# Performance work log

Hardware: AMD Instinct MI355X
Metric: run time of the kernel (lower is better)

Reference implementation:

```python
import jax, jax.numpy as jnp
import numpy as np

N_Q, N_K = 4096, 32768
D_IN_Q, D_IN_V = 1024, 1024
D_QK, D_V = 512, 512
MASK_VAL = -1000.0


def setup_inputs() -> dict:
    key = jax.random.key(0)
    ks = jax.random.split(key, 9)
    X1 = jax.random.normal(ks[0], (N_Q, D_IN_Q), dtype=jnp.float32)
    X2 = jax.random.normal(ks[1], (N_K, D_IN_V), dtype=jnp.float32)
    row_map = jax.random.randint(ks[2], (N_K,), 0, N_Q, dtype=jnp.int32)
    # Linear params (stored as (in, out) for x @ W + b), xavier-ish scale
    def lin(k, din, dout):
        s = jnp.sqrt(6.0 / (din + dout)).astype(jnp.float32)
        return jax.random.uniform(k, (din, dout), jnp.float32, -s, s)
    Wq = lin(ks[3], D_IN_Q, D_QK); bq = jnp.zeros((D_QK,), jnp.float32)
    Wk = lin(ks[4], D_IN_V, D_QK); bk = jnp.zeros((D_QK,), jnp.float32)
    Wv = lin(ks[5], D_IN_V, D_V); bv = jnp.zeros((D_V,), jnp.float32)
    return {"X1": X1, "X2": X2, "Wq": Wq, "bq": bq, "Wk": Wk, "bk": bk,
            "Wv": Wv, "bv": bv, "row_map": row_map}


def reference(X1, X2, Wq, bq, Wk, bk, Wv, bv, row_map):
    n_q = X1.shape[0]
    n_k = X2.shape[0]
    Q = X1 @ Wq + bq                      # (n_q, d_qk)
    K = X2 @ Wk + bk                      # (n_k, d_qk)
    V = X2 @ Wv + bv                      # (n_k, d_v)
    scale = 1.0 / jnp.sqrt(jnp.float32(Q.shape[1]))
    S = (Q @ K.T) * scale                 # (n_q, n_k)
    cols = jnp.arange(n_k)
    # Keep only entries (row_map[j], j); everything else set to -1000 (as in torch)
    S_masked = jnp.full_like(S, MASK_VAL).at[row_map, cols].set(S[row_map, cols])
    W = jax.nn.softmax(S_masked, axis=1)  # (n_q, n_k)
    C = W @ V                             # (n_q, d_v)
    # Queries with no related keys get zero rows (torch skips them entirely)
    counts = jax.ops.segment_sum(jnp.ones((n_k,), jnp.float32), row_map,
                                 num_segments=n_q)
    return jnp.where(counts[:, None] > 0, C, jnp.zeros_like(C))
```

## Files before the change

### kernel.cpp

```cpp
#include <hip/hip_runtime.h>

typedef unsigned short bhalf;
typedef __bf16 bf16x8 __attribute__((ext_vector_type(8)));
typedef float f32x4 __attribute__((ext_vector_type(4)));

#define NQ 4096
#define NK 32768
#define DIN 1024
#define DQK 512
#define CAP 64
#define SCALE 0.044194173824159216f

__device__ __forceinline__ unsigned f2bf(float f) {
  union { float f; unsigned u; } c; c.f = f;
  unsigned u = c.u;
  return (u + 0x7fffu + ((u >> 16) & 1u)) >> 16;
}
__device__ __forceinline__ float bf_lo(unsigned u) {
  union { unsigned u; float f; } c; c.u = u << 16; return c.f;
}
__device__ __forceinline__ float bf_hi(unsigned u) {
  union { unsigned u; float f; } c; c.u = u & 0xffff0000u; return c.f;
}

__global__ __launch_bounds__(256) void prep_kernel(
    const float* __restrict__ Wq, const float* __restrict__ Wk,
    const float* __restrict__ Wv, const float* __restrict__ bq,
    const float* __restrict__ X1, const int* __restrict__ rm,
    bhalf* __restrict__ Wq_b, bhalf* __restrict__ Wk_b, bhalf* __restrict__ WvT,
    bhalf* __restrict__ X1_b,
    float* __restrict__ g_s, int* __restrict__ cnt, int* __restrict__ keyslot) {
  __shared__ float tile[32][33];
  const int b = blockIdx.x;
  const int tid = threadIdx.x;
  if (b < 512) {
    const int bx = b & 15, by = b >> 4;
    const int tx = tid & 31, ty = tid >> 5;
    const int x = bx * 32 + tx;
#pragma unroll
    for (int yy = 0; yy < 32; yy += 8)
      tile[ty + yy][tx] = Wv[(size_t)(by * 32 + ty + yy) * 512 + x];
    __syncthreads();
    const int k = by * 32 + tx;
#pragma unroll
    for (int yy = 0; yy < 32; yy += 8)
      WvT[(size_t)(bx * 32 + ty + yy) * 1024 + k] = (bhalf)f2bf(tile[tx][ty + yy]);
  } else if (b < 768) {
    const int w = (b - 512) * 4 + (tid >> 6);
    const int lane = tid & 63;
    const float* row = Wk + (size_t)w * 512;
    float s = 0.f;
#pragma unroll
    for (int t = 0; t < 2; t++) {
      float4 a = *(const float4*)(row + t * 256 + lane * 4);
      float4 bb2 = *(const float4*)(bq + t * 256 + lane * 4);
      s += a.x * bb2.x + a.y * bb2.y + a.z * bb2.z + a.w * bb2.w;
    }
#pragma unroll
    for (int d = 32; d; d >>= 1) s += __shfl_xor(s, d);
    if (lane == 0) g_s[w] = s * SCALE;
  } else if (b < 1792) {
    const float* in; bhalf* out; int idx;
    if (b < 1280) { in = Wq; out = Wq_b; idx = (b - 768) * 256 + tid; }
    else          { in = Wk; out = Wk_b; idx = (b - 1280) * 256 + tid; }
    float4 v = ((const float4*)in)[idx];
    uint2 o;
    o.x = f2bf(v.x) | (f2bf(v.y) << 16);
    o.y = f2bf(v.z) | (f2bf(v.w) << 16);
    ((uint2*)out)[idx] = o;
  } else if (b < 1920) {
    const int j = (b - 1792) * 256 + tid;
    const int i = rm[j];
    const int p = atomicAdd(&cnt[i], 1);
    if (p < CAP) keyslot[(size_t)i * CAP + p] = j;
  } else {
    const int idx = (b - 1920) * 256 + tid;
    float4 v = ((const float4*)X1)[idx];
    uint2 o;
    o.x = f2bf(v.x) | (f2bf(v.y) << 16);
    o.y = f2bf(v.z) | (f2bf(v.w) << 16);
    ((uint2*)X1_b)[idx] = o;
  }
}

template <int MODE, int MI, int AF32>
__global__ __launch_bounds__(256) void gemm_core(
    const bhalf* __restrict__ A, const float* __restrict__ Afp,
    const bhalf* __restrict__ Bt,
    const float* __restrict__ bias, const int* __restrict__ cnt,
    void* __restrict__ Cout, int M, int N, int K, int nnt) {
  __shared__ __align__(16) bhalf As[MI * 32 * 64];
  __shared__ __align__(16) bhalf Bs[128 * 64];
  const int bid = blockIdx.x;
  const int mt = bid / nnt, nt = bid % nnt;
  const int bmb = mt * (MI * 32), bnb = nt * 128;

  const int tid = threadIdx.x;
  const int lane = tid & 63;
  const int wv = tid >> 6;
  const int wm = (wv & 1) * (MI * 16);
  const int wn = (wv >> 1) * 64;
  const int quad = lane >> 4;
  const int l15 = lane & 15;

  f32x4 acc[MI][4];
#pragma unroll
  for (int i = 0; i < MI; i++)
#pragma unroll
    for (int j = 0; j < 4; j++)
#pragma unroll
      for (int r = 0; r < 4; r++) acc[i][j][r] = 0.0f;

  const int srow = lane >> 3;
  const int scol = (lane & 7) ^ srow;

  for (int kb = 0; kb < K; kb += 64) {
    const size_t goff = (size_t)kb + (size_t)scol * 8;
    if (AF32) {
      const int R = tid >> 2;
      const int q4 = tid & 3;
      const float* arow = Afp + (size_t)(bmb + R) * K + kb + q4 * 16;
      float4 v0 = *(const float4*)(arow + 0);
      float4 v1 = *(const float4*)(arow + 4);
      float4 v2 = *(const float4*)(arow + 8);
      float4 v3 = *(const float4*)(arow + 12);
      uint4 o0, o1;
      o0.x = f2bf(v0.x) | (f2bf(v0.y) << 16);
      o0.y = f2bf(v0.z) | (f2bf(v0.w) << 16);
      o0.z = f2bf(v1.x) | (f2bf(v1.y) << 16);
      o0.w = f2bf(v1.z) | (f2bf(v1.w) << 16);
      o1.x = f2bf(v2.x) | (f2bf(v2.y) << 16);
      o1.y = f2bf(v2.z) | (f2bf(v2.w) << 16);
      o1.z = f2bf(v3.x) | (f2bf(v3.y) << 16);
      o1.w = f2bf(v3.z) | (f2bf(v3.w) << 16);
      const int u0 = q4 * 2, u1 = q4 * 2 + 1;
      *(uint4*)(As + R * 64 + (u0 ^ (R & 7)) * 8) = o0;
      *(uint4*)(As + R * 64 + (u1 ^ (R & 7)) * 8) = o1;
    } else {
#pragma unroll
      for (int r = 0; r < MI; r++) {
        const int chunk = wv * MI + r;
        const int row = chunk * 8 + srow;
        __builtin_amdgcn_global_load_lds(
            (__attribute__((address_space(1))) unsigned int*)(A + (size_t)(bmb + row) * K + goff),
            (__attribute__((address_space(3))) unsigned int*)(As + chunk * 512), 16, 0, 0);
      }
    }
#pragma unroll
    for (int r = 0; r < 4; r++) {
      const int chunk = wv * 4 + r;
      const int row = chunk * 8 + srow;
      __builtin_amdgcn_global_load_lds(
          (__attribute__((address_space(1))) unsigned int*)(Bt + (size_t)(bnb + row) * K + goff),
          (__attribute__((address_space(3))) unsigned int*)(Bs + chunk * 512), 16, 0, 0);
    }
    __syncthreads();
#pragma unroll
    for (int ks = 0; ks < 2; ks++) {
      const int su = ((ks * 4 + quad) ^ (lane & 7)) * 8;
      bf16x8 af[MI], bfr[4];
#pragma unroll
      for (int i = 0; i < MI; i++)
        af[i] = *(const bf16x8*)(As + (wm + i * 16 + l15) * 64 + su);
#pragma unroll
      for (int j = 0; j < 4; j++)
        bfr[j] = *(const bf16x8*)(Bs + (wn + j * 16 + l15) * 64 + su);
#pragma unroll
      for (int i = 0; i < MI; i++)
#pragma unroll
        for (int j = 0; j < 4; j++)
          acc[i][j] = __builtin_amdgcn_mfma_f32_16x16x32_bf16(af[i], bfr[j], acc[i][j], 0, 0, 0);
    }
    __syncthreads();
  }
#pragma unroll
  for (int j = 0; j < 4; j++) {
    const int col = bnb + wn + j * 16 + l15;
    const float bs = (MODE >= 1) ? bias[col] : 0.0f;
#pragma unroll
    for (int i = 0; i < MI; i++) {
#pragma unroll
      for (int r = 0; r < 4; r++) {
        const int row = bmb + wm + i * 16 + quad * 4 + r;
        const float v = acc[i][j][r];
        if (MODE == 0) {
          ((bhalf*)Cout)[(size_t)row * N + col] = (bhalf)f2bf(v * SCALE);
        } else if (MODE == 1) {
          ((bhalf*)Cout)[(size_t)row * N + col] = (bhalf)f2bf(v + bs);
        } else {
          ((float*)Cout)[(size_t)row * N + col] = (cnt[row] > 0) ? (v + bs) : 0.0f;
        }
      }
    }
  }
}

__global__ __launch_bounds__(256) void scorewsum_kernel(
    const bhalf* __restrict__ P, const float* __restrict__ X2,
    const int* __restrict__ cnt, const int* __restrict__ keyslot,
    bhalf* __restrict__ Ub) {
  const int wv = threadIdx.x >> 6;
  const int i = blockIdx.x * 4 + wv;
  const int lane = threadIdx.x & 63;
  int c = cnt[i];
  if (c > CAP) c = CAP;
  const int* klist = keyslot + (size_t)i * CAP;
  const bhalf* Prow = P + (size_t)i * 1024;
  uint4 pb[2];
#pragma unroll
  for (int t = 0; t < 2; t++) pb[t] = *(const uint4*)(Prow + t * 512 + lane * 8);
  float pf[16];
#pragma unroll
  for (int t = 0; t < 2; t++) {
    pf[t * 8 + 0] = bf_lo(pb[t].x); pf[t * 8 + 1] = bf_hi(pb[t].x);
    pf[t * 8 + 2] = bf_lo(pb[t].y); pf[t * 8 + 3] = bf_hi(pb[t].y);
    pf[t * 8 + 4] = bf_lo(pb[t].z); pf[t * 8 + 5] = bf_hi(pb[t].z);
    pf[t * 8 + 6] = bf_lo(pb[t].w); pf[t * 8 + 7] = bf_hi(pb[t].w);
  }

  float sumw = 0.f;
  float4 u[4] = {};
  int pp = 0;
  for (; pp + 2 <= c; pp += 2) {
    const int j0 = klist[pp];
    const int j1 = klist[pp + 1];
    const float* xr0 = X2 + (size_t)j0 * 1024;
    const float* xr1 = X2 + (size_t)j1 * 1024;
    float4 x0[4], x1[4];
#pragma unroll
    for (int t = 0; t < 2; t++) {
      x0[t * 2]     = *(const float4*)(xr0 + t * 512 + lane * 8);
      x0[t * 2 + 1] = *(const float4*)(xr0 + t * 512 + lane * 8 + 4);
      x1[t * 2]     = *(const float4*)(xr1 + t * 512 + lane * 8);
      x1[t * 2 + 1] = *(const float4*)(xr1 + t * 512 + lane * 8 + 4);
    }
    float s0 = 0.f, s1 = 0.f;
#pragma unroll
    for (int t = 0; t < 4; t++) {
      s0 += pf[t * 4 + 0] * x0[t].x + pf[t * 4 + 1] * x0[t].y
          + pf[t * 4 + 2] * x0[t].z + pf[t * 4 + 3] * x0[t].w;
      s1 += pf[t * 4 + 0] * x1[t].x + pf[t * 4 + 1] * x1[t].y
          + pf[t * 4 + 2] * x1[t].z + pf[t * 4 + 3] * x1[t].w;
    }
#pragma unroll
    for (int d = 32; d; d >>= 1) {
      s0 += __shfl_xor(s0, d);
      s1 += __shfl_xor(s1, d);
    }
    const float w0 = __expf(s0);
    const float w1 = __expf(s1);
    sumw += w0 + w1;
#pragma unroll
    for (int t = 0; t < 4; t++) {
      u[t].x += w0 * x0[t].x + w1 * x1[t].x;
      u[t].y += w0 * x0[t].y + w1 * x1[t].y;
      u[t].z += w0 * x0[t].z + w1 * x1[t].z;
      u[t].w += w0 * x0[t].w + w1 * x1[t].w;
    }
  }
  if (pp < c) {
    const int j = klist[pp];
    const float* xr = X2 + (size_t)j * 1024;
    float4 x[4];
#pragma unroll
    for (int t = 0; t < 2; t++) {
      x[t * 2]     = *(const float4*)(xr + t * 512 + lane * 8);
      x[t * 2 + 1] = *(const float4*)(xr + t * 512 + lane * 8 + 4);
    }
    float s = 0.f;
#pragma unroll
    for (int t = 0; t < 4; t++)
      s += pf[t * 4 + 0] * x[t].x + pf[t * 4 + 1] * x[t].y
         + pf[t * 4 + 2] * x[t].z + pf[t * 4 + 3] * x[t].w;
#pragma unroll
    for (int d = 32; d; d >>= 1) s += __shfl_xor(s, d);
    const float w = __expf(s);
    sumw += w;
#pragma unroll
    for (int t = 0; t < 4; t++) {
      u[t].x += w * x[t].x; u[t].y += w * x[t].y;
      u[t].z += w * x[t].z; u[t].w += w * x[t].w;
    }
  }
  const float inv = (c > 0) ? 1.f / sumw : 0.f;
  bhalf* urow = Ub + (size_t)i * 1024;
#pragma unroll
  for (int t = 0; t < 2; t++) {
    uint4 o;
    o.x = f2bf(u[t * 2].x * inv) | (f2bf(u[t * 2].y * inv) << 16);
    o.y = f2bf(u[t * 2].z * inv) | (f2bf(u[t * 2].w * inv) << 16);
    o.z = f2bf(u[t * 2 + 1].x * inv) | (f2bf(u[t * 2 + 1].y * inv) << 16);
    o.w = f2bf(u[t * 2 + 1].z * inv) | (f2bf(u[t * 2 + 1].w * inv) << 16);
    *(uint4*)(urow + t * 512 + lane * 8) = o;
  }
}

extern "C" void kernel_launch(void* const* d_in, const int* in_sizes, int n_in,
                              void* d_out, int out_size, void* d_ws, size_t ws_size,
                              hipStream_t stream) {
  const float* X1 = (const float*)d_in[0];
  const float* X2 = (const float*)d_in[1];
  const float* Wq = (const float*)d_in[2];
  const float* bq = (const float*)d_in[3];
  const float* Wk = (const float*)d_in[4];
  const float* Wv = (const float*)d_in[6];
  const float* bv = (const float*)d_in[7];
  const int* row_map = (const int*)d_in[8];
  float* out = (float*)d_out;

  char* p = (char*)d_ws;
  bhalf* Wq_b = (bhalf*)p; p += (size_t)DIN * DQK * 2;
  bhalf* Wk_b = (bhalf*)p; p += (size_t)DIN * DQK * 2;
  bhalf* WvT  = (bhalf*)p; p += (size_t)DQK * DIN * 2;
  bhalf* Bt2  = (bhalf*)p; p += (size_t)DIN * DIN * 2;
  bhalf* X1_b = (bhalf*)p; p += (size_t)NQ * DIN * 2;
  bhalf* Pbuf = (bhalf*)p; p += (size_t)NQ * DIN * 2;
  bhalf* Ub   = (bhalf*)p; p += (size_t)NQ * DIN * 2;
  float* g_s  = (float*)p; p += DIN * 4;
  int* cnt    = (int*)p;   p += NQ * 4;
  int* keyslot = (int*)p;  p += (size_t)NQ * CAP * 4;

  hipMemsetAsync(cnt, 0, (size_t)NQ * 4, stream);

  prep_kernel<<<6016, 256, 0, stream>>>(Wq, Wk, Wv, bq, X1, row_map,
                                        Wq_b, Wk_b, WvT, X1_b, g_s, cnt, keyslot);

  gemm_core<0, 1, 0><<<256, 256, 0, stream>>>(Wk_b, nullptr, Wq_b, nullptr, nullptr,
                                              Bt2, 1024, 1024, 512, 8);
  gemm_core<1, 2, 0><<<512, 256, 0, stream>>>(X1_b, nullptr, Bt2, g_s, nullptr,
                                              Pbuf, 4096, 1024, 1024, 8);

  scorewsum_kernel<<<NQ / 4, 256, 0, stream>>>(Pbuf, X2, cnt, keyslot, Ub);

  gemm_core<2, 2, 0><<<256, 256, 0, stream>>>(Ub, nullptr, WvT, bv, cnt,
                                              out, 4096, 512, 1024, 4);
}
```

Baseline: 274.3 us.

## Split each query's key loop across four waves with shared-memory reduction

The score/weighted-sum kernel now gives each query row a whole 256-thread block instead of one wave. The four waves take interleaved keys, with key indices preloaded into registers and broadcast by shuffle. Partial sums and weight totals are then combined through shared memory before the bf16 write. This spreads the serial gather-and-reduce over more waves for better latency hiding. The cost is four times more blocks, a block-wide barrier and extra LDS traffic.

```diff
diff --git a/kernel.cpp b/kernel.cpp
--- a/kernel.cpp
+++ b/kernel.cpp
@@ -199,12 +199,22 @@
     const bhalf* __restrict__ P, const float* __restrict__ X2,
     const int* __restrict__ cnt, const int* __restrict__ keyslot,
     bhalf* __restrict__ Ub) {
-  const int wv = threadIdx.x >> 6;
-  const int i = blockIdx.x * 4 + wv;
-  const int lane = threadIdx.x & 63;
+  __shared__ float red[4][1024];
+  __shared__ float sw[4];
+  const int i = blockIdx.x;
+  const int tid = threadIdx.x;
+  const int wv = tid >> 6;
+  const int lane = tid & 63;
   int c = cnt[i];
   if (c > CAP) c = CAP;
   const int* klist = keyslot + (size_t)i * CAP;
+
+  int jreg = 0;
+  if (lane < 16) {
+    const int slot = wv + 4 * lane;
+    if (slot < c) jreg = klist[slot];
+  }
+
   const bhalf* Prow = P + (size_t)i * 1024;
   uint4 pb[2];
 #pragma unroll
@@ -220,79 +230,51 @@
 
   float sumw = 0.f;
   float4 u[4] = {};
-  int pp = 0;
-  for (; pp + 2 <= c; pp += 2) {
-    const int j0 = klist[pp];
-    const int j1 = klist[pp + 1];
-    const float* xr0 = X2 + (size_t)j0 * 1024;
-    const float* xr1 = X2 + (size_t)j1 * 1024;
-    float4 x0[4], x1[4];
-#pragma unroll
-    for (int t = 0; t < 2; t++) {
-      x0[t * 2]     = *(const float4*)(xr0 + t * 512 + lane * 8);
-      x0[t * 2 + 1] = *(const float4*)(xr0 + t * 512 + lane * 8 + 4);
-      x1[t * 2]     = *(const float4*)(xr1 + t * 512 + lane * 8);
-      x1[t * 2 + 1] = *(const float4*)(xr1 + t * 512 + lane * 8 + 4);
-    }
-    float s0 = 0.f, s1 = 0.f;
-#pragma unroll
-    for (int t = 0; t < 4; t++) {
-      s0 += pf[t * 4 + 0] * x0[t].x + pf[t * 4 + 1] * x0[t].y
-          + pf[t * 4 + 2] * x0[t].z + pf[t * 4 + 3] * x0[t].w;
-      s1 += pf[t * 4 + 0] * x1[t].x + pf[t * 4 + 1] * x1[t].y
-          + pf[t * 4 + 2] * x1[t].z + pf[t * 4 + 3] * x1[t].w;
-    }
-#pragma unroll
-    for (int d = 32; d; d >>= 1) {
-      s0 += __shfl_xor(s0, d);
-      s1 += __shfl_xor(s1, d);
-    }
-    const float w0 = __expf(s0);
-    const float w1 = __expf(s1);
-    sumw += w0 + w1;
-#pragma unroll
-    for (int t = 0; t < 4; t++) {
-      u[t].x += w0 * x0[t].x + w1 * x1[t].x;
-      u[t].y += w0 * x0[t].y + w1 * x1[t].y;
-      u[t].z += w0 * x0[t].z + w1 * x1[t].z;
-      u[t].w += w0 * x0[t].w + w1 * x1[t].w;
-    }
-  }
-  if (pp < c) {
-    const int j = klist[pp];
+  const int nit = (c > wv) ? ((c - wv + 3) >> 2) : 0;
+  for (int t = 0; t < nit; t++) {
+    const int j = __shfl(jreg, t);
     const float* xr = X2 + (size_t)j * 1024;
     float4 x[4];
-#pragma unroll
-    for (int t = 0; t < 2; t++) {
-      x[t * 2]     = *(const float4*)(xr + t * 512 + lane * 8);
-      x[t * 2 + 1] = *(const float4*)(xr + t * 512 + lane * 8 + 4);
-    }
+    x[0] = *(const float4*)(xr + lane * 8);
+    x[1] = *(const float4*)(xr + lane * 8 + 4);
+    x[2] = *(const float4*)(xr + 512 + lane * 8);
+    x[3] = *(const float4*)(xr + 512 + lane * 8 + 4);
     float s = 0.f;
 #pragma unroll
-    for (int t = 0; t < 4; t++)
-      s += pf[t * 4 + 0] * x[t].x + pf[t * 4 + 1] * x[t].y
-         + pf[t * 4 + 2] * x[t].z + pf[t * 4 + 3] * x[t].w;
+    for (int tt = 0; tt < 4; tt++)
+      s += pf[tt * 4 + 0] * x[tt].x + pf[tt * 4 + 1] * x[tt].y
+         + pf[tt * 4 + 2] * x[tt].z + pf[tt * 4 + 3] * x[tt].w;
 #pragma unroll
     for (int d = 32; d; d >>= 1) s += __shfl_xor(s, d);
     const float w = __expf(s);
     sumw += w;
 #pragma unroll
-    for (int t = 0; t < 4; t++) {
-      u[t].x += w * x[t].x; u[t].y += w * x[t].y;
-      u[t].z += w * x[t].z; u[t].w += w * x[t].w;
-    }
-  }
-  const float inv = (c > 0) ? 1.f / sumw : 0.f;
-  bhalf* urow = Ub + (size_t)i * 1024;
-#pragma unroll
-  for (int t = 0; t < 2; t++) {
-    uint4 o;
-    o.x = f2bf(u[t * 2].x * inv) | (f2bf(u[t * 2].y * inv) << 16);
-    o.y = f2bf(u[t * 2].z * inv) | (f2bf(u[t * 2].w * inv) << 16);
-    o.z = f2bf(u[t * 2 + 1].x * inv) | (f2bf(u[t * 2 + 1].y * inv) << 16);
-    o.w = f2bf(u[t * 2 + 1].z * inv) | (f2bf(u[t * 2 + 1].w * inv) << 16);
-    *(uint4*)(urow + t * 512 + lane * 8) = o;
-  }
+    for (int tt = 0; tt < 4; tt++) {
+      u[tt].x += w * x[tt].x; u[tt].y += w * x[tt].y;
+      u[tt].z += w * x[tt].z; u[tt].w += w * x[tt].w;
+    }
+  }
+
+  *(float4*)&red[wv][lane * 8]       = u[0];
+  *(float4*)&red[wv][lane * 8 + 4]   = u[1];
+  *(float4*)&red[wv][512 + lane * 8]     = u[2];
+  *(float4*)&red[wv][512 + lane * 8 + 4] = u[3];
+  if (lane == 0) sw[wv] = sumw;
+  __syncthreads();
+  const float tot = sw[0] + sw[1] + sw[2] + sw[3];
+  const float inv = (c > 0) ? 1.f / tot : 0.f;
+  const float4 a0 = *(const float4*)&red[0][tid * 4];
+  const float4 a1 = *(const float4*)&red[1][tid * 4];
+  const float4 a2 = *(const float4*)&red[2][tid * 4];
+  const float4 a3 = *(const float4*)&red[3][tid * 4];
+  const float vx = (a0.x + a1.x + a2.x + a3.x) * inv;
+  const float vy = (a0.y + a1.y + a2.y + a3.y) * inv;
+  const float vz = (a0.z + a1.z + a2.z + a3.z) * inv;
+  const float vw = (a0.w + a1.w + a2.w + a3.w) * inv;
+  uint2 o;
+  o.x = f2bf(vx) | (f2bf(vy) << 16);
+  o.y = f2bf(vz) | (f2bf(vw) << 16);
+  ((uint2*)(Ub + (size_t)i * 1024))[tid] = o;
 }
 
 extern "C" void kernel_launch(void* const* d_in, const int* in_sizes, int n_in,
@@ -330,7 +312,7 @@
   gemm_core<1, 2, 0><<<512, 256, 0, stream>>>(X1_b, nullptr, Bt2, g_s, nullptr,
                                               Pbuf, 4096, 1024, 1024, 8);
 
-  scorewsum_kernel<<<NQ / 4, 256, 0, stream>>>(Pbuf, X2, cnt, keyslot, Ub);
+  scorewsum_kernel<<<NQ, 256, 0, stream>>>(Pbuf, X2, cnt, keyslot, Ub);
 
   gemm_core<2, 2, 0><<<256, 256, 0, stream>>>(Ub, nullptr, WvT, bv, cnt,
                                               out, 4096, 512, 1024, 4);
```

After: 275.2 us. Within noise of the previous version (+0.3%).
